# Kernel tuning notes

Measured on AMD Instinct MI355X. Metric: run time of the kernel, lower is better.

The kernel has to match this reference:

```python
import jax, jax.numpy as jnp
import numpy as np

B, I, T, O = 256, 182, 2000, 2


def setup_inputs() -> dict:
    key = jax.random.key(0)
    k1, k2, k3, k4, k5 = jax.random.split(key, 5)
    inputs = jax.random.uniform(k1, (B, I, T), dtype=jnp.float32)  # [batch, input_dim, steps]
    W = jax.random.normal(k2, (O, I), dtype=jnp.float32) / np.sqrt(I)
    b = jax.random.normal(k3, (O,), dtype=jnp.float32) * 0.01
    alpha = jax.random.uniform(k4, (O,), dtype=jnp.float32)  # synaptic decay
    beta = jax.random.uniform(k5, (O,), dtype=jnp.float32)   # membrane decay
    return {"inputs": inputs, "W": W, "b": b, "alpha": alpha, "beta": beta}


def reference(inputs, W, b, alpha, beta):
    # SNN branch of DecoderSVM.forward with bin_width_ms//DT == 1 (record mem every step).
    # snntorch Synaptic (reset_mechanism='none'):
    #   syn_t = clamp(alpha,0,1)*syn_{t-1} + curr_t
    #   mem_t = clamp(beta,0,1)*mem_{t-1} + syn_t
    # Spikes are computed but unused since mem_rec records the membrane voltage.
    a = jnp.clip(alpha, 0.0, 1.0)
    bta = jnp.clip(beta, 0.0, 1.0)
    # Precompute all per-step currents in one GEMM: [T, B, O]
    curr = jnp.einsum('bit,oi->tbo', inputs, W) + b

    def step(carry, c):
        syn, mem = carry
        syn = a * syn + c
        mem = bta * mem + syn
        return (syn, mem), mem

    z = jnp.zeros((inputs.shape[0], W.shape[0]), dtype=inputs.dtype)
    _, mem_rec = jax.lax.scan(step, (z, z), curr)  # [T, B, O]
    return jnp.transpose(mem_rec, (1, 0, 2))  # [B, T, O]
```

## Files before the change

kernel.cpp:

```cpp
#include <hip/hip_runtime.h>
#include <hip/hip_bf16.h>

#define BB 256
#define II 182
#define TT 2000
#define OO 2

__global__ __launch_bounds__(256) void curr_kernel(const float* __restrict__ in,
                                                   const float* __restrict__ W,
                                                   const float* __restrict__ bias,
                                                   float* __restrict__ curr) {
    __shared__ float w0[II];
    __shared__ float w1[II];
    for (int i = threadIdx.x; i < II; i += blockDim.x) {
        w0[i] = W[i];
        w1[i] = W[II + i];
    }
    __syncthreads();

    const int b = blockIdx.x >> 1;
    const int g = (blockIdx.x & 1) * blockDim.x + threadIdx.x;
    if (g >= TT / 4) return;
    const int t = g * 4;

    const float4* p = (const float4*)(in + (size_t)b * II * TT + t);
    const int stride4 = TT / 4;

    float4 acc0 = {0.f, 0.f, 0.f, 0.f};
    float4 acc1 = {0.f, 0.f, 0.f, 0.f};

#pragma unroll 2
    for (int i = 0; i < II; ++i) {
        const float4 x = p[(size_t)i * stride4];
        const float a = w0[i];
        const float c = w1[i];
        acc0.x += x.x * a; acc0.y += x.y * a; acc0.z += x.z * a; acc0.w += x.w * a;
        acc1.x += x.x * c; acc1.y += x.y * c; acc1.z += x.z * c; acc1.w += x.w * c;
    }

    const float b0 = bias[0];
    const float b1 = bias[1];
    acc0.x += b0; acc0.y += b0; acc0.z += b0; acc0.w += b0;
    acc1.x += b1; acc1.y += b1; acc1.z += b1; acc1.w += b1;

    float4* c0 = (float4*)(curr + ((size_t)b * OO + 0) * TT + t);
    float4* c1 = (float4*)(curr + ((size_t)b * OO + 1) * TT + t);
    *c0 = acc0;
    *c1 = acc1;
}

__global__ __launch_bounds__(64) void scan_kernel(const float* __restrict__ curr,
                                                  const float* __restrict__ alpha,
                                                  const float* __restrict__ beta,
                                                  float* __restrict__ out) {
    const int gid = blockIdx.x * 64 + threadIdx.x;
    if (gid >= BB * OO) return;
    const int b = gid >> 1;
    const int o = gid & 1;

    const float a  = fminf(fmaxf(alpha[o], 0.f), 1.f);
    const float bt = fminf(fmaxf(beta[o],  0.f), 1.f);

    const float4* c4 = (const float4*)(curr + ((size_t)b * OO + o) * TT);
    float* op = out + (size_t)b * TT * OO + o;

    float syn = 0.f, mem = 0.f;
    for (int t4 = 0; t4 < TT / 4; ++t4) {
        const float4 x = c4[t4];
        const int tb = t4 * 4;
        syn = a * syn + x.x; mem = bt * mem + syn; op[(tb + 0) * OO] = mem;
        syn = a * syn + x.y; mem = bt * mem + syn; op[(tb + 1) * OO] = mem;
        syn = a * syn + x.z; mem = bt * mem + syn; op[(tb + 2) * OO] = mem;
        syn = a * syn + x.w; mem = bt * mem + syn; op[(tb + 3) * OO] = mem;
    }
}

extern "C" void kernel_launch(void* const* d_in, const int* in_sizes, int n_in,
                              void* d_out, int out_size, void* d_ws, size_t ws_size,
                              hipStream_t stream) {
    const float* inputs = (const float*)d_in[0];
    const float* W      = (const float*)d_in[1];
    const float* bias   = (const float*)d_in[2];
    const float* alpha  = (const float*)d_in[3];
    const float* beta   = (const float*)d_in[4];
    float* out = (float*)d_out;
    float* curr = (float*)d_ws;

    curr_kernel<<<BB * 2, 256, 0, stream>>>(inputs, W, bias, curr);

    scan_kernel<<<(BB * OO + 63) / 64, 64, 0, stream>>>(curr, alpha, beta, out);
}
```

Baseline: 586.0 us.

## Fuse current GEMV and recurrent scan into one per-batch kernel via LDS

Merges the two kernels into a single kernel with one 512-thread block per batch row. Each block computes the currents into shared memory, runs the serial scan on two threads, stages the membrane trace in LDS and writes it out with coalesced float4 stores. This removes the global round-trip for the intermediate currents, a second launch, and the strided scalar output stores. The trade-off is that the serial scan now runs on only two lanes per block while the other threads sit idle, and the large LDS footprint limits occupancy.

```diff
diff --git a/kernel.cpp b/kernel.cpp
--- a/kernel.cpp
+++ b/kernel.cpp
@@ -6,72 +6,70 @@
 #define TT 2000
 #define OO 2
 
-__global__ __launch_bounds__(256) void curr_kernel(const float* __restrict__ in,
-                                                   const float* __restrict__ W,
-                                                   const float* __restrict__ bias,
-                                                   float* __restrict__ curr) {
+__global__ __launch_bounds__(512) void snn_fused_kernel(const float* __restrict__ in,
+                                                        const float* __restrict__ W,
+                                                        const float* __restrict__ bias,
+                                                        const float* __restrict__ alpha,
+                                                        const float* __restrict__ beta,
+                                                        float* __restrict__ out) {
     __shared__ float w0[II];
     __shared__ float w1[II];
-    for (int i = threadIdx.x; i < II; i += blockDim.x) {
-        w0[i] = W[i];
-        w1[i] = W[II + i];
+    __shared__ float curr_s[OO][TT];
+    __shared__ float mem_s[TT * OO];
+
+    const int b = blockIdx.x;
+    const int tid = threadIdx.x;
+
+    if (tid < II) {
+        w0[tid] = W[tid];
+        w1[tid] = W[II + tid];
     }
     __syncthreads();
 
-    const int b = blockIdx.x >> 1;
-    const int g = (blockIdx.x & 1) * blockDim.x + threadIdx.x;
-    if (g >= TT / 4) return;
-    const int t = g * 4;
+    if (tid < TT / 4) {
+        const float4* p = (const float4*)(in + (size_t)b * II * TT) + tid;
+        float4 a0 = {0.f, 0.f, 0.f, 0.f};
+        float4 a1 = {0.f, 0.f, 0.f, 0.f};
+#pragma unroll 7
+        for (int i = 0; i < II; ++i) {
+            const float4 x = p[i * (TT / 4)];
+            const float wa = w0[i];
+            const float wb = w1[i];
+            a0.x += x.x * wa; a0.y += x.y * wa; a0.z += x.z * wa; a0.w += x.w * wa;
+            a1.x += x.x * wb; a1.y += x.y * wb; a1.z += x.z * wb; a1.w += x.w * wb;
+        }
+        const float b0 = bias[0];
+        const float b1 = bias[1];
+        const int t = tid * 4;
+        curr_s[0][t + 0] = a0.x + b0; curr_s[0][t + 1] = a0.y + b0;
+        curr_s[0][t + 2] = a0.z + b0; curr_s[0][t + 3] = a0.w + b0;
+        curr_s[1][t + 0] = a1.x + b1; curr_s[1][t + 1] = a1.y + b1;
+        curr_s[1][t + 2] = a1.z + b1; curr_s[1][t + 3] = a1.w + b1;
+    }
+    __syncthreads();
 
-    const float4* p = (const float4*)(in + (size_t)b * II * TT + t);
-    const int stride4 = TT / 4;
+    if (tid < OO) {
+        const int o = tid;
+        const float a  = fminf(fmaxf(alpha[o], 0.f), 1.f);
+        const float bt = fminf(fmaxf(beta[o],  0.f), 1.f);
+        const float4* c4 = (const float4*)curr_s[o];
+        float syn = 0.f, mem = 0.f;
+        for (int t4 = 0; t4 < TT / 4; ++t4) {
+            const float4 x = c4[t4];
+            const int t = t4 * 4;
+            syn = a * syn + x.x; mem = bt * mem + syn; mem_s[(t + 0) * OO + o] = mem;
+            syn = a * syn + x.y; mem = bt * mem + syn; mem_s[(t + 1) * OO + o] = mem;
+            syn = a * syn + x.z; mem = bt * mem + syn; mem_s[(t + 2) * OO + o] = mem;
+            syn = a * syn + x.w; mem = bt * mem + syn; mem_s[(t + 3) * OO + o] = mem;
+        }
+    }
+    __syncthreads();
 
-    float4 acc0 = {0.f, 0.f, 0.f, 0.f};
-    float4 acc1 = {0.f, 0.f, 0.f, 0.f};
-
-#pragma unroll 2
-    for (int i = 0; i < II; ++i) {
-        const float4 x = p[(size_t)i * stride4];
-        const float a = w0[i];
-        const float c = w1[i];
-        acc0.x += x.x * a; acc0.y += x.y * a; acc0.z += x.z * a; acc0.w += x.w * a;
-        acc1.x += x.x * c; acc1.y += x.y * c; acc1.z += x.z * c; acc1.w += x.w * c;
-    }
-
-    const float b0 = bias[0];
-    const float b1 = bias[1];
-    acc0.x += b0; acc0.y += b0; acc0.z += b0; acc0.w += b0;
-    acc1.x += b1; acc1.y += b1; acc1.z += b1; acc1.w += b1;
-
-    float4* c0 = (float4*)(curr + ((size_t)b * OO + 0) * TT + t);
-    float4* c1 = (float4*)(curr + ((size_t)b * OO + 1) * TT + t);
-    *c0 = acc0;
-    *c1 = acc1;
-}
-
-__global__ __launch_bounds__(64) void scan_kernel(const float* __restrict__ curr,
-                                                  const float* __restrict__ alpha,
-                                                  const float* __restrict__ beta,
-                                                  float* __restrict__ out) {
-    const int gid = blockIdx.x * 64 + threadIdx.x;
-    if (gid >= BB * OO) return;
-    const int b = gid >> 1;
-    const int o = gid & 1;
-
-    const float a  = fminf(fmaxf(alpha[o], 0.f), 1.f);
-    const float bt = fminf(fmaxf(beta[o],  0.f), 1.f);
-
-    const float4* c4 = (const float4*)(curr + ((size_t)b * OO + o) * TT);
-    float* op = out + (size_t)b * TT * OO + o;
-
-    float syn = 0.f, mem = 0.f;
-    for (int t4 = 0; t4 < TT / 4; ++t4) {
-        const float4 x = c4[t4];
-        const int tb = t4 * 4;
-        syn = a * syn + x.x; mem = bt * mem + syn; op[(tb + 0) * OO] = mem;
-        syn = a * syn + x.y; mem = bt * mem + syn; op[(tb + 1) * OO] = mem;
-        syn = a * syn + x.z; mem = bt * mem + syn; op[(tb + 2) * OO] = mem;
-        syn = a * syn + x.w; mem = bt * mem + syn; op[(tb + 3) * OO] = mem;
+    float4* o4 = (float4*)(out + (size_t)b * TT * OO);
+    const float4* m4 = (const float4*)mem_s;
+#pragma unroll
+    for (int idx = tid; idx < TT * OO / 4; idx += 512) {
+        o4[idx] = m4[idx];
     }
 }
 
@@ -84,9 +82,6 @@
     const float* alpha  = (const float*)d_in[3];
     const float* beta   = (const float*)d_in[4];
     float* out = (float*)d_out;
-    float* curr = (float*)d_ws;
 
-    curr_kernel<<<BB * 2, 256, 0, stream>>>(inputs, W, bias, curr);
-
-    scan_kernel<<<(BB * OO + 63) / 64, 64, 0, stream>>>(curr, alpha, beta, out);
+    snn_fused_kernel<<<BB, 512, 0, stream>>>(inputs, W, bias, alpha, beta, out);
 }
```

Result: faster. 513.0 us (-12.5%).
